# Optimization experiments

Measured on AMD Instinct MI355X. Metric: run time of the kernel, lower is better.

The kernel has to match this reference:

```python
import jax, jax.numpy as jnp
import numpy as np

CAL_LIST = ["+", "-", "*", "/", "sin", "cos", "exp", "log", "square"]
MAX_MLT = 99999999.0   # overflow cap for * and square
MAX_DIV = 9999.0       # overflow cap for /
MAX_EXP = 17.0         # cap on exp argument
MIN_DENOM = 0.0001     # added to exactly-zero denominators


def _clip_mag(v, mx):
    # Replicates: tmp = abs(mx / v) under no_grad; v * tmp where |v| >= mx
    scale = jax.lax.stop_gradient(jnp.abs(mx / v))
    return jnp.where(jnp.abs(v) >= mx, v * scale, v)


def _apply_ops(x2):
    # x2: [B, variDim]; consumes 2 cols per binary op, 1 per unary op.
    outs = []
    s = 0
    for op in CAL_LIST:
        if op in ("+", "-", "*", "/"):
            a, b = x2[:, s], x2[:, s + 1]
            s += 2
        else:
            a = x2[:, s]
            s += 1
        if op == "+":
            o = a + b
        elif op == "-":
            o = a - b
        elif op == "*":
            o = _clip_mag(a * b, MAX_MLT)
        elif op == "/":
            denom = jnp.where(b == 0.0, b + MIN_DENOM, b)
            o = _clip_mag(a / denom, MAX_DIV)
        elif op == "sin":
            o = jnp.sin(a)
        elif op == "cos":
            o = jnp.cos(a)
        elif op == "exp":
            safe = jnp.where(a >= MAX_EXP, a * jax.lax.stop_gradient(MAX_EXP / a), a)
            o = jnp.exp(safe)
        elif op == "log":
            o = jnp.log(jnp.abs(a))
        elif op == "square":
            o = _clip_mag(a * a, MAX_MLT)
        outs.append(o)
    return jnp.stack(outs, axis=1)  # [B, calNum]


def setup_inputs() -> dict:
    key = jax.random.key(0)
    B = 524288
    vari_num, const_num = 4, 4
    cal_num = len(CAL_LIST)            # 9
    vari_dim = 13                      # sum(opNumList)
    n_layers = 8
    ks = jax.random.split(key, n_layers + 2)
    x = jax.random.normal(ks[0], (B, vari_num + const_num), dtype=jnp.float32)
    inp = {"x": x}
    in_dim = vari_num + const_num
    for i in range(n_layers):
        inp[f"W{i+1}"] = 0.1 * jax.random.normal(ks[i + 1], (vari_dim, in_dim), dtype=jnp.float32)
        in_dim += cal_num              # concat of op outputs with layer input
    inp["Wf"] = 0.1 * jax.random.normal(ks[-1], (1, in_dim), dtype=jnp.float32)
    return inp


def reference(x, W1, W2, W3, W4, W5, W6, W7, W8, Wf):
    h = x
    for W in (W1, W2, W3, W4, W5, W6, W7, W8):
        z = h @ W.T                      # [B, variDim]
        h = jnp.concatenate([_apply_ops(z), h], axis=1)
    return h @ Wf.T                      # [B, 1]
```

## Files before the change

kernel.cpp:

```cpp
#include <hip/hip_runtime.h>
#include <math.h>


static constexpr double MAX_MLT   = 99999999.0;
static constexpr double MAX_DIV   = 9999.0;
static constexpr double MAX_EXP_C = 17.0;
static constexpr double MIN_DENOM = 0.0001;

static constexpr int IN0  = 8;
static constexpr int VDIM = 13;
static constexpr int NOPS = 9;
static constexpr int FDIM = 80;

static constexpr int WSZ[9]  = {104, 221, 338, 455, 572, 689, 806, 923, 80};
static constexpr int WOFF[9] = {0, 104, 325, 663, 1118, 1690, 2379, 3185, 4108};

__global__ void widen_kernel(const float* __restrict__ s0, const float* __restrict__ s1,
                             const float* __restrict__ s2, const float* __restrict__ s3,
                             const float* __restrict__ s4, const float* __restrict__ s5,
                             const float* __restrict__ s6, const float* __restrict__ s7,
                             const float* __restrict__ s8, double* __restrict__ dst) {
    int seg = blockIdx.y;
    int i   = blockIdx.x * blockDim.x + threadIdx.x;
    const float* src;
    switch (seg) {
        case 0: src = s0; break; case 1: src = s1; break; case 2: src = s2; break;
        case 3: src = s3; break; case 4: src = s4; break; case 5: src = s5; break;
        case 6: src = s6; break; case 7: src = s7; break; default: src = s8; break;
    }
    if (i < WSZ[seg]) dst[WOFF[seg] + i] = (double)src[i];
}

struct D2 { double s, c; };
__device__ __attribute__((noinline))
D2 d_sincos2(double as, double ac) {
    D2 r;
    r.s = sin(as);
    r.c = cos(ac);
    return r;
}

__device__ __forceinline__ double clip_ref(double v, double mx) {
    double scale = fabs(mx / v);
    double vs    = v * scale;
    return (fabs(v) >= mx) ? vs : v;
}

template<int IN_DIM, int BASE>
__device__ __forceinline__ void layer_step(const double* __restrict__ W,
                                           double (&h)[FDIM]) {
    double z[VDIM];
    #pragma unroll 2
    for (int j = 0; j < VDIM; ++j) {
        const double* Wr = W + j * IN_DIM;
        double acc = 0.0;
        #pragma unroll
        for (int k = 0; k < IN_DIM; ++k) {
            acc = fma(Wr[k], h[BASE + k], acc);
        }
        z[j] = acc;
    }
    constexpr int BO = BASE - NOPS;
    h[BO + 0] = z[0] + z[1];
    h[BO + 1] = z[2] - z[3];
    h[BO + 2] = clip_ref(z[4] * z[5], MAX_MLT);
    {
        double b     = z[7];
        double denom = (b == 0.0) ? (b + MIN_DENOM) : b;
        h[BO + 3]    = clip_ref(z[6] / denom, MAX_DIV);
    }
    {
        D2 t = d_sincos2(z[8], z[9]);
        h[BO + 4] = t.s;
        h[BO + 5] = t.c;
    }
    {
        double a    = z[10];
        double safe = (a >= MAX_EXP_C) ? (a * (MAX_EXP_C / a)) : a;
        h[BO + 6]   = exp(safe);
    }
    h[BO + 7] = log(fabs(z[11]));
    h[BO + 8] = clip_ref(z[12] * z[12], MAX_MLT);
}

__global__ void __launch_bounds__(64)
net_kernel(const float* __restrict__ x, const double* __restrict__ Wd,
           float* __restrict__ out, int nrows) {
    int row = blockIdx.x * blockDim.x + threadIdx.x;
    if (row >= nrows) return;

    double h[FDIM];

    const float4* x4 = reinterpret_cast<const float4*>(x);
    float4 xa = x4[row * 2 + 0];
    float4 xb = x4[row * 2 + 1];
    h[72] = (double)xa.x; h[73] = (double)xa.y; h[74] = (double)xa.z; h[75] = (double)xa.w;
    h[76] = (double)xb.x; h[77] = (double)xb.y; h[78] = (double)xb.z; h[79] = (double)xb.w;

    layer_step<IN0 + 0 * NOPS, 72>(Wd + WOFF[0], h);
    layer_step<IN0 + 1 * NOPS, 63>(Wd + WOFF[1], h);
    layer_step<IN0 + 2 * NOPS, 54>(Wd + WOFF[2], h);
    layer_step<IN0 + 3 * NOPS, 45>(Wd + WOFF[3], h);
    layer_step<IN0 + 4 * NOPS, 36>(Wd + WOFF[4], h);
    layer_step<IN0 + 5 * NOPS, 27>(Wd + WOFF[5], h);
    layer_step<IN0 + 6 * NOPS, 18>(Wd + WOFF[6], h);
    layer_step<IN0 + 7 * NOPS,  9>(Wd + WOFF[7], h);

    const double* Wf = Wd + WOFF[8];
    double acc = 0.0;
    #pragma unroll
    for (int k = 0; k < FDIM; ++k) {
        acc = fma(Wf[k], h[k], acc);
    }
    out[row] = (float)acc;
}

extern "C" void kernel_launch(void* const* d_in, const int* in_sizes, int n_in,
                              void* d_out, int out_size, void* d_ws, size_t ws_size,
                              hipStream_t stream) {
    const float* x = (const float*)d_in[0];
    double* Wd     = (double*)d_ws;
    float* out     = (float*)d_out;

    {
        dim3 grid((923 + 255) / 256, 9);
        widen_kernel<<<grid, 256, 0, stream>>>(
            (const float*)d_in[1], (const float*)d_in[2], (const float*)d_in[3],
            (const float*)d_in[4], (const float*)d_in[5], (const float*)d_in[6],
            (const float*)d_in[7], (const float*)d_in[8], (const float*)d_in[9],
            Wd);
    }

    int nrows = in_sizes[0] / IN0;
    int block = 64;
    int grid  = (nrows + block - 1) / block;
    net_kernel<<<grid, block, 0, stream>>>(x, Wd, out, nrows);
}
```

Measured before the change: 274.8 us.

## Process two rows per thread to share weight loads across rows

```diff
diff --git a/kernel.cpp b/kernel.cpp
--- a/kernel.cpp
+++ b/kernel.cpp
@@ -46,21 +46,8 @@
     return (fabs(v) >= mx) ? vs : v;
 }
 
-template<int IN_DIM, int BASE>
-__device__ __forceinline__ void layer_step(const double* __restrict__ W,
-                                           double (&h)[FDIM]) {
-    double z[VDIM];
-    #pragma unroll 2
-    for (int j = 0; j < VDIM; ++j) {
-        const double* Wr = W + j * IN_DIM;
-        double acc = 0.0;
-        #pragma unroll
-        for (int k = 0; k < IN_DIM; ++k) {
-            acc = fma(Wr[k], h[BASE + k], acc);
-        }
-        z[j] = acc;
-    }
-    constexpr int BO = BASE - NOPS;
+template<int BO>
+__device__ __forceinline__ void ops_row(const double (&z)[VDIM], double (&h)[FDIM]) {
     h[BO + 0] = z[0] + z[1];
     h[BO + 1] = z[2] - z[3];
     h[BO + 2] = clip_ref(z[4] * z[5], MAX_MLT);
@@ -83,36 +70,70 @@
     h[BO + 8] = clip_ref(z[12] * z[12], MAX_MLT);
 }
 
-__global__ void __launch_bounds__(64)
+template<int IN_DIM, int BASE>
+__device__ __forceinline__ void layer_step2(const double* __restrict__ W,
+                                            double (&hA)[FDIM], double (&hB)[FDIM]) {
+    double zA[VDIM], zB[VDIM];
+    #pragma unroll 2
+    for (int j = 0; j < VDIM; ++j) {
+        const double* Wr = W + j * IN_DIM;
+        double aA = 0.0, aB = 0.0;
+        #pragma unroll
+        for (int k = 0; k < IN_DIM; ++k) {
+            double w = Wr[k];
+            aA = fma(w, hA[BASE + k], aA);
+            aB = fma(w, hB[BASE + k], aB);
+        }
+        zA[j] = aA;
+        zB[j] = aB;
+    }
+    constexpr int BO = BASE - NOPS;
+    ops_row<BO>(zA, hA);
+    ops_row<BO>(zB, hB);
+}
+
+__global__ void __launch_bounds__(64, 1)
 net_kernel(const float* __restrict__ x, const double* __restrict__ Wd,
            float* __restrict__ out, int nrows) {
-    int row = blockIdx.x * blockDim.x + threadIdx.x;
-    if (row >= nrows) return;
+    int half = nrows >> 1;
+    int tid  = blockIdx.x * blockDim.x + threadIdx.x;
+    bool active = tid < half;
+    int rA = active ? tid : 0;
+    int rB = rA + half;
 
-    double h[FDIM];
+    double hA[FDIM], hB[FDIM];
 
     const float4* x4 = reinterpret_cast<const float4*>(x);
-    float4 xa = x4[row * 2 + 0];
-    float4 xb = x4[row * 2 + 1];
-    h[72] = (double)xa.x; h[73] = (double)xa.y; h[74] = (double)xa.z; h[75] = (double)xa.w;
-    h[76] = (double)xb.x; h[77] = (double)xb.y; h[78] = (double)xb.z; h[79] = (double)xb.w;
+    {
+        float4 a0 = x4[rA * 2 + 0], a1 = x4[rA * 2 + 1];
+        hA[72] = (double)a0.x; hA[73] = (double)a0.y; hA[74] = (double)a0.z; hA[75] = (double)a0.w;
+        hA[76] = (double)a1.x; hA[77] = (double)a1.y; hA[78] = (double)a1.z; hA[79] = (double)a1.w;
+        float4 b0 = x4[rB * 2 + 0], b1 = x4[rB * 2 + 1];
+        hB[72] = (double)b0.x; hB[73] = (double)b0.y; hB[74] = (double)b0.z; hB[75] = (double)b0.w;
+        hB[76] = (double)b1.x; hB[77] = (double)b1.y; hB[78] = (double)b1.z; hB[79] = (double)b1.w;
+    }
 
-    layer_step<IN0 + 0 * NOPS, 72>(Wd + WOFF[0], h);
-    layer_step<IN0 + 1 * NOPS, 63>(Wd + WOFF[1], h);
-    layer_step<IN0 + 2 * NOPS, 54>(Wd + WOFF[2], h);
-    layer_step<IN0 + 3 * NOPS, 45>(Wd + WOFF[3], h);
-    layer_step<IN0 + 4 * NOPS, 36>(Wd + WOFF[4], h);
-    layer_step<IN0 + 5 * NOPS, 27>(Wd + WOFF[5], h);
-    layer_step<IN0 + 6 * NOPS, 18>(Wd + WOFF[6], h);
-    layer_step<IN0 + 7 * NOPS,  9>(Wd + WOFF[7], h);
+    layer_step2<IN0 + 0 * NOPS, 72>(Wd + WOFF[0], hA, hB);
+    layer_step2<IN0 + 1 * NOPS, 63>(Wd + WOFF[1], hA, hB);
+    layer_step2<IN0 + 2 * NOPS, 54>(Wd + WOFF[2], hA, hB);
+    layer_step2<IN0 + 3 * NOPS, 45>(Wd + WOFF[3], hA, hB);
+    layer_step2<IN0 + 4 * NOPS, 36>(Wd + WOFF[4], hA, hB);
+    layer_step2<IN0 + 5 * NOPS, 27>(Wd + WOFF[5], hA, hB);
+    layer_step2<IN0 + 6 * NOPS, 18>(Wd + WOFF[6], hA, hB);
+    layer_step2<IN0 + 7 * NOPS,  9>(Wd + WOFF[7], hA, hB);
 
     const double* Wf = Wd + WOFF[8];
-    double acc = 0.0;
+    double accA = 0.0, accB = 0.0;
     #pragma unroll
     for (int k = 0; k < FDIM; ++k) {
-        acc = fma(Wf[k], h[k], acc);
+        double w = Wf[k];
+        accA = fma(w, hA[k], accA);
+        accB = fma(w, hB[k], accB);
     }
-    out[row] = (float)acc;
+    if (active) {
+        out[rA] = (float)accA;
+        out[rB] = (float)accB;
+    }
 }
 
 extern "C" void kernel_launch(void* const* d_in, const int* in_sizes, int n_in,
@@ -132,7 +153,8 @@
     }
 
     int nrows = in_sizes[0] / IN0;
+    int half  = nrows / 2;
     int block = 64;
-    int grid  = (nrows + block - 1) / block;
+    int grid  = (half + block - 1) / block;
     net_kernel<<<grid, block, 0, stream>>>(x, Wd, out, nrows);
 }
```

Measured after the change: 554.1 us. 2.02x slower.
